# Optimization experiments

Measured on AMD Instinct MI355X. Metric: run time of the kernel, lower is better.

The kernel has to match this reference:

```python
import jax, jax.numpy as jnp
import numpy as np

B, N_WIRES, LAYERS = 256, 14, 3


def _apply_1q(psi, U, w, n):
    # U: [2,2] (shared across batch) or [B,2,2] (per-sample) complex gate on wire w.
    # Wire 0 is the most-significant tensor factor (PennyLane convention).
    Bsz = psi.shape[0]
    p = psi.reshape(Bsz, 2 ** w, 2, 2 ** (n - w - 1))
    sub = 'bij,bljr->blir' if U.ndim == 3 else 'ij,bljr->blir'
    return jnp.einsum(sub, U, p).reshape(Bsz, -1)


def _apply_rz(psi, theta, w, n):
    # RZ is diagonal: multiply by exp(-i*theta/2), exp(+i*theta/2) on wire w.
    Bsz = psi.shape[0]
    p = psi.reshape(Bsz, 2 ** w, 2, 2 ** (n - w - 1))
    ph = jnp.stack([jnp.exp(-0.5j * theta), jnp.exp(0.5j * theta)])
    return (p * ph[None, None, :, None]).reshape(Bsz, -1)


def _apply_cnot(psi, c, n):
    # CNOT on adjacent wires (control=c, target=c+1): flip target where control=1.
    Bsz = psi.shape[0]
    p = psi.reshape(Bsz, 2 ** c, 2, 2, 2 ** (n - c - 2))
    p = jnp.concatenate([p[:, :, 0:1], p[:, :, 1:2, ::-1]], axis=2)
    return p.reshape(Bsz, -1)


def _circuit(state_batch, var_params):
    Bsz, n = state_batch.shape
    layers = var_params.shape[0]
    psi = jnp.zeros((Bsz, 2 ** n), jnp.complex64).at[:, 0].set(1.0)
    # --- RX encoding with per-sample angles ---
    half = 0.5 * state_batch
    c = jnp.cos(half).astype(jnp.complex64)
    s = (-1j) * jnp.sin(half).astype(jnp.complex64)
    for w in range(n):
        U = jnp.stack([jnp.stack([c[:, w], s[:, w]], -1),
                       jnp.stack([s[:, w], c[:, w]], -1)], -2)  # [B,2,2]
        psi = _apply_1q(psi, U, w, n)
    # --- variational layers: RY, RZ per wire, then CNOT chain ---
    for l in range(layers):
        for w in range(n):
            a = var_params[l, w, 0]
            ca, sa = jnp.cos(0.5 * a), jnp.sin(0.5 * a)
            RY = jnp.stack([jnp.stack([ca, -sa]),
                            jnp.stack([sa, ca])]).astype(jnp.complex64)
            psi = _apply_1q(psi, RY, w, n)
            psi = _apply_rz(psi, var_params[l, w, 1], w, n)
        for i in range(n - 1):
            psi = _apply_cnot(psi, i, n)
    # --- <Z_w> for each wire via signed probability sums ---
    probs = (psi * jnp.conj(psi)).real  # [B, 2^n]
    bits = (np.arange(2 ** n)[None, :] >> (n - 1 - np.arange(n))[:, None]) & 1
    signs = jnp.asarray(1.0 - 2.0 * bits, dtype=probs.dtype)  # [n, 2^n]
    return probs @ signs.T  # [B, n]


def setup_inputs() -> dict:
    key = jax.random.key(0)
    k1, k2, k3 = jax.random.split(key, 3)
    return {
        'state_batch': jax.random.normal(k1, (B, N_WIRES), dtype=jnp.float32),
        'var_params': jax.random.normal(k2, (LAYERS, N_WIRES, 3), dtype=jnp.float32),
        'head_w': jax.random.normal(k3, (1, N_WIRES), dtype=jnp.float32) * 0.25,
        'head_b': jnp.zeros((1,), dtype=jnp.float32),
    }


def reference(state_batch, var_params, head_w, head_b):
    z = _circuit(state_batch, var_params)          # [B, n] PauliZ expectations
    return (z @ head_w.T + head_b)[:, 0]           # Linear(n,1).squeeze(-1) -> [B]
```

## Files before the change

### kernel.cpp

```cpp
#include <hip/hip_runtime.h>


#define NW      14
#define NSTATE  (1 << NW)
#define TPB     1024
#define NLAYERS 3
#define NGATES  (NLAYERS * NW)

typedef float v2f __attribute__((ext_vector_type(2)));

__device__ __forceinline__ int swz(int i) {
    return i ^ ((i >> 4) & 15) ^ ((i >> 8) & 15) ^ ((i >> 9) & 16);
}
__device__ __forceinline__ v2f vswp(v2f a) { return __builtin_shufflevector(a, a, 1, 0); }
__device__ __forceinline__ v2f vspl(float x) { v2f r; r.x = x;  r.y = x; return r; }
__device__ __forceinline__ v2f vpm(float x)  { v2f r; r.x = -x; r.y = x; return r; }
__device__ __forceinline__ float rfl(float x) {
    return __int_as_float(__builtin_amdgcn_readfirstlane(__float_as_int(x)));
}
__device__ __forceinline__ v2f cml(v2f a, v2f b) {
    return vspl(a.x) * b + vpm(a.y) * vswp(b);
}
template <int CTRL>
__device__ __forceinline__ v2f dpp2(v2f a) {
    v2f r;
    r.x = __int_as_float(__builtin_amdgcn_update_dpp(
              0, __float_as_int(a.x), CTRL, 0xF, 0xF, true));
    r.y = __int_as_float(__builtin_amdgcn_update_dpp(
              0, __float_as_int(a.y), CTRL, 0xF, 0xF, true));
    return r;
}

__device__ __forceinline__ void pgp(v2f& a, v2f& d,
                                    float x00, float y00, float x01, float y01,
                                    float x10, float y10, float x11, float y11) {
    const v2f sa = vswp(a), sd = vswp(d);
    const v2f na = vspl(x00) * a + vpm(y00) * sa + vspl(x01) * d + vpm(y01) * sd;
    const v2f nd = vspl(x10) * a + vpm(y10) * sa + vspl(x11) * d + vpm(y11) * sd;
    a = na; d = nd;
}
__device__ __forceinline__ void pgr(v2f& a, v2f& d,
                                    float x00, float x01, float x10, float x11) {
    const v2f na = vspl(x00) * a + vspl(x01) * d;
    const v2f nd = vspl(x10) * a + vspl(x11) * d;
    a = na; d = nd;
}

#define GATE_SGPR(pre, g) \
    const float4 pre##A = gt4[2*(g)], pre##B = gt4[2*(g)+1]; \
    const float pre##0 = rfl(pre##A.x), pre##1 = rfl(pre##A.y), \
                pre##2 = rfl(pre##A.z), pre##3 = rfl(pre##A.w), \
                pre##4 = rfl(pre##B.x), pre##5 = rfl(pre##B.y), \
                pre##6 = rfl(pre##B.z), pre##7 = rfl(pre##B.w);

#define PGP(a, d, pre) pgp(a, d, pre##0,pre##1,pre##2,pre##3, pre##4,pre##5,pre##6,pre##7)
#define PGR(a, d, pre) pgr(a, d, pre##0,pre##2,pre##4,pre##6)

#define LGC1(aX, CT) { const v2f p_ = dpp2<CT>(aX); \
    aX = vspl(cox)*aX + vpm(coy)*vswp(aX) + vspl(cpx)*p_ + vpm(cpy)*vswp(p_); }
#define LGC_ALL(CT) \
    LGC1(a0,CT) LGC1(a1,CT) LGC1(a2,CT) LGC1(a3,CT) \
    LGC1(a4,CT) LGC1(a5,CT) LGC1(a6,CT) LGC1(a7,CT) \
    LGC1(a8,CT) LGC1(a9,CT) LGC1(aA,CT) LGC1(aB,CT) \
    LGC1(aC,CT) LGC1(aD,CT) LGC1(aE,CT) LGC1(aF,CT)
#define LGR1(aX, CT) { const v2f p_ = dpp2<CT>(aX); \
    aX = vspl(cor)*aX + vspl(cpr)*p_; }
#define LGR_ALL(CT) \
    LGR1(a0,CT) LGR1(a1,CT) LGR1(a2,CT) LGR1(a3,CT) \
    LGR1(a4,CT) LGR1(a5,CT) LGR1(a6,CT) LGR1(a7,CT) \
    LGR1(a8,CT) LGR1(a9,CT) LGR1(aA,CT) LGR1(aB,CT) \
    LGR1(aC,CT) LGR1(aD,CT) LGR1(aE,CT) LGR1(aF,CT)

#define MEAS(aX, Dn, par) { \
    const float m_ = ((Dn)&8?-h8:h8)+((Dn)&4?-h9:h9)+((Dn)&2?-h10:h10)+((Dn)&1?-h11:h11); \
    const float cf_ = coefHigh + sc*m_ + ((par)? -Wp : Wp); \
    acc += (aX.x*aX.x + aX.y*aX.y)*cf_; }

__global__ void __launch_bounds__(TPB)
qsim_kernel(const float* __restrict__ state_batch,
            const float* __restrict__ var_params,
            const float* __restrict__ head_w,
            const float* __restrict__ head_b,
            float* __restrict__ out)
{
    __shared__ v2f    psi[NSTATE];
    __shared__ float4 gt4[NGATES * 2];
    __shared__ v2f    vws[NW][2];
    __shared__ float  hws[NW];
    __shared__ float  red[TPB / 64];

    const int t    = threadIdx.x;
    const int lane = t & 63;
    const int wave = t >> 6;
    const int b    = blockIdx.x;

    if (t < NW) {
        float sx, cx, sy, cy, sz, cz;
        sincosf(0.5f * state_batch[b * NW + t], &sx, &cx);
        sincosf(0.5f * var_params[t * 3 + 0], &sy, &cy);
        sincosf(0.5f * var_params[t * 3 + 1], &sz, &cz);
        const float tr = cy * cx, ti = sy * sx;
        const float br = sy * cx, bi = -cy * sx;
        v2f v0, v1;
        v0.x = cz * tr + sz * ti;  v0.y = cz * ti - sz * tr;
        v1.x = cz * br - sz * bi;  v1.y = cz * bi + sz * br;
        vws[t][0] = v0; vws[t][1] = v1;
    }
    if (t >= 64 && t < 64 + NGATES) {
        const int g = t - 64;
        if (g >= NW) {
            float sa, ca, sz, cz;
            sincosf(0.5f * var_params[g * 3 + 0], &sa, &ca);
            if (g >= 2 * NW) { sz = 0.f; cz = 1.f; }
            else sincosf(0.5f * var_params[g * 3 + 1], &sz, &cz);
            gt4[2*g]   = make_float4( ca * cz, -ca * sz, -sa * cz,  sa * sz);
            gt4[2*g+1] = make_float4( sa * cz,  sa * sz,  ca * cz,  ca * sz);
        }
    }
    if (t >= 128 && t < 128 + NW) hws[t - 128] = head_w[t - 128];
    __syncthreads();

    float acc = 0.f;

#pragma unroll 1
    for (int l = 1; l < NLAYERS; ++l) {
        const int g0 = l * NW;
#pragma unroll 1
        for (int p = 0; p < 3; ++p) {
            const int SB = 10 - 4 * p;
            const int LO = 1 << SB;
            const int S0 = swz(LO), S1 = swz(LO << 1);
            const int S2 = swz(LO << 2), S3 = swz(LO << 3);
            const int M  = S3 ^ S2 ^ S1 ^ S0;
            const int gw = g0 + 4 * p;
            GATE_SGPR(ga, gw); GATE_SGPR(gb, gw + 1);
            GATE_SGPR(gc, gw + 2); GATE_SGPR(gd, gw + 3);

            const int i0 = ((t >> SB) << (SB + 4)) | (t & (LO - 1));
            const int s  = swz(i0);

            v2f a0, a1, a2, a3, a4, a5, a6, a7;
            v2f a8, a9, aA, aB, aC, aD, aE, aF;
            if (l == 1 && p == 0) {
                v2f base = cml(vws[5][((t >> 8) ^ (t >> 9)) & 1],
                               vws[6][((t >> 7) ^ (t >> 8)) & 1]);
                v2f m2   = cml(vws[7][((t >> 6) ^ (t >> 7)) & 1],
                               vws[8][((t >> 5) ^ (t >> 6)) & 1]);
                v2f m3   = cml(vws[9][((t >> 4) ^ (t >> 5)) & 1],
                               vws[10][((t >> 3) ^ (t >> 4)) & 1]);
                v2f m4   = cml(vws[11][((t >> 2) ^ (t >> 3)) & 1],
                               vws[12][((t >> 1) ^ (t >> 2)) & 1]);
                base = cml(base, m2);
                m3   = cml(m3, m4);
                base = cml(base, m3);
                base = cml(base, vws[13][(t ^ (t >> 1)) & 1]);
                const int t9 = (t >> 9) & 1;
                const v2f B0 = cml(base, vws[4][t9]);
                const v2f B1 = cml(base, vws[4][t9 ^ 1]);
                const v2f w3B00 = cml(vws[3][0], B0);
                const v2f w3B01 = cml(vws[3][1], B1);
                const v2f w3B10 = cml(vws[3][1], B0);
                const v2f w3B11 = cml(vws[3][0], B1);
                v2f p_, t20, t21;
                p_ = cml(vws[0][0], vws[1][0]);
                t20 = cml(p_, vws[2][0]); t21 = cml(p_, vws[2][1]);
                a0 = cml(t20, w3B00); a1 = cml(t20, w3B01);
                a2 = cml(t21, w3B10); a3 = cml(t21, w3B11);
                p_ = cml(vws[0][0], vws[1][1]);
                t20 = cml(p_, vws[2][1]); t21 = cml(p_, vws[2][0]);
                a4 = cml(t20, w3B00); a5 = cml(t20, w3B01);
                a6 = cml(t21, w3B10); a7 = cml(t21, w3B11);
                p_ = cml(vws[0][1], vws[1][1]);
                t20 = cml(p_, vws[2][0]); t21 = cml(p_, vws[2][1]);
                a8 = cml(t20, w3B00); a9 = cml(t20, w3B01);
                aA = cml(t21, w3B10); aB = cml(t21, w3B11);
                p_ = cml(vws[0][1], vws[1][0]);
                t20 = cml(p_, vws[2][1]); t21 = cml(p_, vws[2][0]);
                aC = cml(t20, w3B00); aD = cml(t20, w3B01);
                aE = cml(t21, w3B10); aF = cml(t21, w3B11);
            } else {
                a0 = psi[s];                a1 = psi[s ^ S0];
                a2 = psi[s ^ S1];           a3 = psi[s ^ S1 ^ S0];
                a4 = psi[s ^ S2];           a5 = psi[s ^ S2 ^ S0];
                a6 = psi[s ^ S2 ^ S1];      a7 = psi[s ^ S2 ^ S1 ^ S0];
                a8 = psi[s ^ S3];           a9 = psi[s ^ S3 ^ S0];
                aA = psi[s ^ S3 ^ S1];      aB = psi[s ^ S3 ^ S1 ^ S0];
                aC = psi[s ^ S3 ^ S2];      aD = psi[s ^ S3 ^ S2 ^ S0];
                aE = psi[s ^ S3 ^ S2 ^ S1]; aF = psi[s ^ M];
            }

            if (l < NLAYERS - 1) {
                PGP(a0, a8, ga); PGP(a1, a9, ga); PGP(a2, aA, ga); PGP(a3, aB, ga);
                PGP(a4, aC, ga); PGP(a5, aD, ga); PGP(a6, aE, ga); PGP(a7, aF, ga);
                PGP(a0, a4, gb); PGP(a1, a5, gb); PGP(a2, a6, gb); PGP(a3, a7, gb);
                PGP(a8, aC, gb); PGP(a9, aD, gb); PGP(aA, aE, gb); PGP(aB, aF, gb);
                PGP(a0, a2, gc); PGP(a1, a3, gc); PGP(a4, a6, gc); PGP(a5, a7, gc);
                PGP(a8, aA, gc); PGP(a9, aB, gc); PGP(aC, aE, gc); PGP(aD, aF, gc);
                PGP(a0, a1, gd); PGP(a2, a3, gd); PGP(a4, a5, gd); PGP(a6, a7, gd);
                PGP(a8, a9, gd); PGP(aA, aB, gd); PGP(aC, aD, gd); PGP(aE, aF, gd);
            } else {
                PGR(a0, a8, ga); PGR(a1, a9, ga); PGR(a2, aA, ga); PGR(a3, aB, ga);
                PGR(a4, aC, ga); PGR(a5, aD, ga); PGR(a6, aE, ga); PGR(a7, aF, ga);
                PGR(a0, a4, gb); PGR(a1, a5, gb); PGR(a2, a6, gb); PGR(a3, a7, gb);
                PGR(a8, aC, gb); PGR(a9, aD, gb); PGR(aA, aE, gb); PGR(aB, aF, gb);
                PGR(a0, a2, gc); PGR(a1, a3, gc); PGR(a4, a6, gc); PGR(a5, a7, gc);
                PGR(a8, aA, gc); PGR(a9, aB, gc); PGR(aC, aE, gc); PGR(aD, aF, gc);
                PGR(a0, a1, gd); PGR(a2, a3, gd); PGR(a4, a5, gd); PGR(a6, a7, gd);
                PGR(a8, a9, gd); PGR(aA, aB, gd); PGR(aC, aD, gd); PGR(aE, aF, gd);
            }

            if (p < 2) {
                const bool cs = ((t >> SB) & 1) != 0;
                const int e = s ^ (cs ? M : 0);
                psi[e]                = a0; psi[e ^ S0]           = a1;
                psi[e ^ S1 ^ S0]      = a2; psi[e ^ S1]           = a3;
                psi[e ^ S2 ^ S1 ^ S0] = a4; psi[e ^ S2 ^ S1]      = a5;
                psi[e ^ S2]           = a6; psi[e ^ S2 ^ S0]      = a7;
                psi[e ^ M]            = a8; psi[e ^ S3 ^ S2 ^ S1] = a9;
                psi[e ^ S3 ^ S2]      = aA; psi[e ^ S3 ^ S2 ^ S0] = aB;
                psi[e ^ S3]           = aC; psi[e ^ S3 ^ S0]      = aD;
                psi[e ^ S3 ^ S1 ^ S0] = aE; psi[e ^ S3 ^ S1]      = aF;
                __syncthreads();
            } else if (l < NLAYERS - 1) {
                GATE_SGPR(gu, g0 + 12);
                GATE_SGPR(gv, g0 + 13);
                {
                    const bool hi = (t & 2) != 0;
                    const float cox = hi ? gu6 : gu0, coy = hi ? gu7 : gu1;
                    const float cpx = hi ? gu4 : gu2, cpy = hi ? gu5 : gu3;
                    LGC_ALL(0x4E)
                }
                {
                    const bool hi = (t & 1) != 0;
                    const float cox = hi ? gv6 : gv0, coy = hi ? gv7 : gv1;
                    const float cpx = hi ? gv4 : gv2, cpy = hi ? gv5 : gv3;
                    LGC_ALL(0xB1)
                }
                const bool cs = ((t >> SB) & 1) != 0;
                const int e = s ^ (cs ? (M ^ 3) : 0) ^ ((t >> 1) & 1);
                psi[e]                    = a0; psi[e ^ S0 ^ 3]           = a1;
                psi[e ^ S1 ^ S0 ^ 3]      = a2; psi[e ^ S1]               = a3;
                psi[e ^ S2 ^ S1 ^ S0 ^ 3] = a4; psi[e ^ S2 ^ S1]          = a5;
                psi[e ^ S2]               = a6; psi[e ^ S2 ^ S0 ^ 3]      = a7;
                psi[e ^ M ^ 3]            = a8; psi[e ^ S3 ^ S2 ^ S1]     = a9;
                psi[e ^ S3 ^ S2]          = aA; psi[e ^ S3 ^ S2 ^ S0 ^ 3] = aB;
                psi[e ^ S3]               = aC; psi[e ^ S3 ^ S0 ^ 3]      = aD;
                psi[e ^ S3 ^ S1 ^ S0 ^ 3] = aE; psi[e ^ S3 ^ S1]          = aF;
                __syncthreads();
            } else {
                GATE_SGPR(gu, g0 + 12);
                GATE_SGPR(gv, g0 + 13);
                {
                    const float cor = gu0;
                    const float cpr = (t & 2) ? gu4 : gu2;
                    LGR_ALL(0x4E)
                }
                {
                    const float cor = gv0;
                    const float cpr = (t & 1) ? gv4 : gv2;
                    LGR_ALL(0xB1)
                }
                const float h8 = hws[8], h9 = hws[9], h10 = hws[10], h11 = hws[11];
                const float h12 = hws[12], h13 = hws[13];
                float coefHigh = 0.f;
#pragma unroll
                for (int j = 0; j < 8; ++j)
                    coefHigh += ((t >> (9 - j)) & 1) ? -hws[j] : hws[j];
                const bool cs = ((t >> SB) & 1) != 0;
                const float sc = cs ? -1.f : 1.f;
                const float w12_0 = (t & 2) ? -h12 : h12;
                const float w13_0 = (((t >> 1) ^ t) & 1) ? -h13 : h13;
                const float Ssum = w12_0 + w13_0;
                const float Wp = cs ? -Ssum : Ssum;
                MEAS(a0, 0, 0)  MEAS(a1, 1, 1)  MEAS(a2, 3, 1)  MEAS(a3, 2, 0)
                MEAS(a4, 7, 1)  MEAS(a5, 6, 0)  MEAS(a6, 4, 0)  MEAS(a7, 5, 1)
                MEAS(a8, 15, 1) MEAS(a9, 14, 0) MEAS(aA, 12, 0) MEAS(aB, 13, 1)
                MEAS(aC, 8, 0)  MEAS(aD, 9, 1)  MEAS(aE, 11, 1) MEAS(aF, 10, 0)
            }
        }
    }

#pragma unroll
    for (int off = 32; off > 0; off >>= 1)
        acc += __shfl_down(acc, off, 64);
    if (lane == 0) red[wave] = acc;
    __syncthreads();
    if (t == 0) {
        float s = 0.f;
#pragma unroll
        for (int i = 0; i < TPB / 64; ++i) s += red[i];
        out[b] = s + head_b[0];
    }
}

extern "C" void kernel_launch(void* const* d_in, const int* in_sizes, int n_in,
                              void* d_out, int out_size, void* d_ws, size_t ws_size,
                              hipStream_t stream) {
    const float* state_batch = (const float*)d_in[0];
    const float* var_params  = (const float*)d_in[1];
    const float* head_w      = (const float*)d_in[2];
    const float* head_b      = (const float*)d_in[3];
    float* out = (float*)d_out;
    qsim_kernel<<<dim3(out_size), dim3(TPB), 0, stream>>>(
        state_batch, var_params, head_w, head_b, out);
}
```

Before: 81.73 us.

## Split fused RY·RZ gates into real RY rotations plus batched diagonal phases

Layer 1's fused complex RY·RZ gate is replaced by a real RY butterfly followed by one combined diagonal phase per amplitude. The phase comes from precomputed tables covering the four wires of each pass, plus a separate table for wires 12 and 13. Because RZ is diagonal and commutes past later RY gates on other wires, the product of RZ phases is applied once per amplitude instead of per gate. This roughly halves the FLOPs of the butterflies but adds extra LDS table reads and per-amplitude complex multiplies, and it relies on the RZ/CNOT ordering being preserved.

```diff
diff --git a/kernel.cpp b/kernel.cpp
--- a/kernel.cpp
+++ b/kernel.cpp
@@ -5,7 +5,6 @@
 #define NSTATE  (1 << NW)
 #define TPB     1024
 #define NLAYERS 3
-#define NGATES  (NLAYERS * NW)
 
 typedef float v2f __attribute__((ext_vector_type(2)));
 
@@ -30,15 +29,6 @@
               0, __float_as_int(a.y), CTRL, 0xF, 0xF, true));
     return r;
 }
-
-__device__ __forceinline__ void pgp(v2f& a, v2f& d,
-                                    float x00, float y00, float x01, float y01,
-                                    float x10, float y10, float x11, float y11) {
-    const v2f sa = vswp(a), sd = vswp(d);
-    const v2f na = vspl(x00) * a + vpm(y00) * sa + vspl(x01) * d + vpm(y01) * sd;
-    const v2f nd = vspl(x10) * a + vpm(y10) * sa + vspl(x11) * d + vpm(y11) * sd;
-    a = na; d = nd;
-}
 __device__ __forceinline__ void pgr(v2f& a, v2f& d,
                                     float x00, float x01, float x10, float x11) {
     const v2f na = vspl(x00) * a + vspl(x01) * d;
@@ -46,23 +36,19 @@
     a = na; d = nd;
 }
 
-#define GATE_SGPR(pre, g) \
-    const float4 pre##A = gt4[2*(g)], pre##B = gt4[2*(g)+1]; \
-    const float pre##0 = rfl(pre##A.x), pre##1 = rfl(pre##A.y), \
-                pre##2 = rfl(pre##A.z), pre##3 = rfl(pre##A.w), \
-                pre##4 = rfl(pre##B.x), pre##5 = rfl(pre##B.y), \
-                pre##6 = rfl(pre##B.z), pre##7 = rfl(pre##B.w);
-
-#define PGP(a, d, pre) pgp(a, d, pre##0,pre##1,pre##2,pre##3, pre##4,pre##5,pre##6,pre##7)
-#define PGR(a, d, pre) pgr(a, d, pre##0,pre##2,pre##4,pre##6)
-
-#define LGC1(aX, CT) { const v2f p_ = dpp2<CT>(aX); \
-    aX = vspl(cox)*aX + vpm(coy)*vswp(aX) + vspl(cpx)*p_ + vpm(cpy)*vswp(p_); }
-#define LGC_ALL(CT) \
-    LGC1(a0,CT) LGC1(a1,CT) LGC1(a2,CT) LGC1(a3,CT) \
-    LGC1(a4,CT) LGC1(a5,CT) LGC1(a6,CT) LGC1(a7,CT) \
-    LGC1(a8,CT) LGC1(a9,CT) LGC1(aA,CT) LGC1(aB,CT) \
-    LGC1(aC,CT) LGC1(aD,CT) LGC1(aE,CT) LGC1(aF,CT)
+#define GATE_R(pre, g) \
+    const float4 pre##V = gtr[g]; \
+    const float pre##0 = rfl(pre##V.x), pre##1 = rfl(pre##V.y), \
+                pre##2 = rfl(pre##V.z), pre##3 = rfl(pre##V.w);
+#define PGR4(a, d, pre) pgr(a, d, pre##0, pre##1, pre##2, pre##3)
+
+#define PH2(aE, aO, k) { \
+    const float4 Z_ = zph4[zb + (k)]; \
+    const float ex_ = rfl(Z_.x), ey_ = rfl(Z_.y); \
+    const float ox_ = rfl(Z_.z), oy_ = rfl(Z_.w); \
+    aE = vspl(ex_)*aE + vpm(ey_)*vswp(aE); \
+    aO = vspl(ox_)*aO + vpm(oy_)*vswp(aO); }
+
 #define LGR1(aX, CT) { const v2f p_ = dpp2<CT>(aX); \
     aX = vspl(cor)*aX + vspl(cpr)*p_; }
 #define LGR_ALL(CT) \
@@ -70,6 +56,11 @@
     LGR1(a4,CT) LGR1(a5,CT) LGR1(a6,CT) LGR1(a7,CT) \
     LGR1(a8,CT) LGR1(a9,CT) LGR1(aA,CT) LGR1(aB,CT) \
     LGR1(aC,CT) LGR1(aD,CT) LGR1(aE,CT) LGR1(aF,CT)
+
+#define ETA(aX) { aX = vspl(et.x)*aX + vpm(et.y)*vswp(aX); }
+#define ETA_ALL \
+    ETA(a0) ETA(a1) ETA(a2) ETA(a3) ETA(a4) ETA(a5) ETA(a6) ETA(a7) \
+    ETA(a8) ETA(a9) ETA(aA) ETA(aB) ETA(aC) ETA(aD) ETA(aE) ETA(aF)
 
 #define MEAS(aX, Dn, par) { \
     const float m_ = ((Dn)&8?-h8:h8)+((Dn)&4?-h9:h9)+((Dn)&2?-h10:h10)+((Dn)&1?-h11:h11); \
@@ -84,7 +75,9 @@
             float* __restrict__ out)
 {
     __shared__ v2f    psi[NSTATE];
-    __shared__ float4 gt4[NGATES * 2];
+    __shared__ float4 gtr[2 * NW];
+    __shared__ float4 zph4[3 * 8];
+    __shared__ v2f    zph12[4];
     __shared__ v2f    vws[NW][2];
     __shared__ float  hws[NW];
     __shared__ float  red[TPB / 64];
@@ -106,25 +99,42 @@
         v1.x = cz * br - sz * bi;  v1.y = cz * bi + sz * br;
         vws[t][0] = v0; vws[t][1] = v1;
     }
-    if (t >= 64 && t < 64 + NGATES) {
+    if (t >= 64 && t < 64 + 2 * NW) {
         const int g = t - 64;
-        if (g >= NW) {
-            float sa, ca, sz, cz;
-            sincosf(0.5f * var_params[g * 3 + 0], &sa, &ca);
-            if (g >= 2 * NW) { sz = 0.f; cz = 1.f; }
-            else sincosf(0.5f * var_params[g * 3 + 1], &sz, &cz);
-            gt4[2*g]   = make_float4( ca * cz, -ca * sz, -sa * cz,  sa * sz);
-            gt4[2*g+1] = make_float4( sa * cz,  sa * sz,  ca * cz,  ca * sz);
+        float sa, ca;
+        sincosf(0.5f * var_params[(NW + g) * 3 + 0], &sa, &ca);
+        gtr[g] = make_float4(ca, -sa, sa, ca);
+    }
+    if (t >= 128 && t < 128 + NW) hws[t - 128] = head_w[t - 128];
+    if (t >= 192 && t < 240) {
+        const int k = t - 192, p = k >> 4, o = k & 15;
+        float ang = 0.f;
+#pragma unroll
+        for (int j = 0; j < 4; ++j) {
+            const float z = var_params[(NW + 4 * p + j) * 3 + 1];
+            ang += ((o >> (3 - j)) & 1) ? 0.5f * z : -0.5f * z;
         }
-    }
-    if (t >= 128 && t < 128 + NW) hws[t - 128] = head_w[t - 128];
+        float s_, c_; sincosf(ang, &s_, &c_);
+        if (o & 1) { zph4[p * 8 + (o >> 1)].z = c_; zph4[p * 8 + (o >> 1)].w = s_; }
+        else       { zph4[p * 8 + (o >> 1)].x = c_; zph4[p * 8 + (o >> 1)].y = s_; }
+    }
+    if (t >= 240 && t < 244) {
+        const int k2 = t - 240;
+        const float z12 = var_params[(NW + 12) * 3 + 1];
+        const float z13 = var_params[(NW + 13) * 3 + 1];
+        const float ang = ((k2 & 2) ? 0.5f * z12 : -0.5f * z12)
+                        + ((k2 & 1) ? 0.5f * z13 : -0.5f * z13);
+        float s_, c_; sincosf(ang, &s_, &c_);
+        v2f e; e.x = c_; e.y = s_;
+        zph12[k2] = e;
+    }
     __syncthreads();
 
     float acc = 0.f;
 
 #pragma unroll 1
     for (int l = 1; l < NLAYERS; ++l) {
-        const int g0 = l * NW;
+        const int gl = (l - 1) * NW;
 #pragma unroll 1
         for (int p = 0; p < 3; ++p) {
             const int SB = 10 - 4 * p;
@@ -132,9 +142,9 @@
             const int S0 = swz(LO), S1 = swz(LO << 1);
             const int S2 = swz(LO << 2), S3 = swz(LO << 3);
             const int M  = S3 ^ S2 ^ S1 ^ S0;
-            const int gw = g0 + 4 * p;
-            GATE_SGPR(ga, gw); GATE_SGPR(gb, gw + 1);
-            GATE_SGPR(gc, gw + 2); GATE_SGPR(gd, gw + 3);
+            const int zb = p * 8;
+            GATE_R(ga, gl + 4 * p);     GATE_R(gb, gl + 4 * p + 1);
+            GATE_R(gc, gl + 4 * p + 2); GATE_R(gd, gl + 4 * p + 3);
 
             const int i0 = ((t >> SB) << (SB + 4)) | (t & (LO - 1));
             const int s  = swz(i0);
@@ -189,24 +199,18 @@
                 aE = psi[s ^ S3 ^ S2 ^ S1]; aF = psi[s ^ M];
             }
 
-            if (l < NLAYERS - 1) {
-                PGP(a0, a8, ga); PGP(a1, a9, ga); PGP(a2, aA, ga); PGP(a3, aB, ga);
-                PGP(a4, aC, ga); PGP(a5, aD, ga); PGP(a6, aE, ga); PGP(a7, aF, ga);
-                PGP(a0, a4, gb); PGP(a1, a5, gb); PGP(a2, a6, gb); PGP(a3, a7, gb);
-                PGP(a8, aC, gb); PGP(a9, aD, gb); PGP(aA, aE, gb); PGP(aB, aF, gb);
-                PGP(a0, a2, gc); PGP(a1, a3, gc); PGP(a4, a6, gc); PGP(a5, a7, gc);
-                PGP(a8, aA, gc); PGP(a9, aB, gc); PGP(aC, aE, gc); PGP(aD, aF, gc);
-                PGP(a0, a1, gd); PGP(a2, a3, gd); PGP(a4, a5, gd); PGP(a6, a7, gd);
-                PGP(a8, a9, gd); PGP(aA, aB, gd); PGP(aC, aD, gd); PGP(aE, aF, gd);
-            } else {
-                PGR(a0, a8, ga); PGR(a1, a9, ga); PGR(a2, aA, ga); PGR(a3, aB, ga);
-                PGR(a4, aC, ga); PGR(a5, aD, ga); PGR(a6, aE, ga); PGR(a7, aF, ga);
-                PGR(a0, a4, gb); PGR(a1, a5, gb); PGR(a2, a6, gb); PGR(a3, a7, gb);
-                PGR(a8, aC, gb); PGR(a9, aD, gb); PGR(aA, aE, gb); PGR(aB, aF, gb);
-                PGR(a0, a2, gc); PGR(a1, a3, gc); PGR(a4, a6, gc); PGR(a5, a7, gc);
-                PGR(a8, aA, gc); PGR(a9, aB, gc); PGR(aC, aE, gc); PGR(aD, aF, gc);
-                PGR(a0, a1, gd); PGR(a2, a3, gd); PGR(a4, a5, gd); PGR(a6, a7, gd);
-                PGR(a8, a9, gd); PGR(aA, aB, gd); PGR(aC, aD, gd); PGR(aE, aF, gd);
+            PGR4(a0, a8, ga); PGR4(a1, a9, ga); PGR4(a2, aA, ga); PGR4(a3, aB, ga);
+            PGR4(a4, aC, ga); PGR4(a5, aD, ga); PGR4(a6, aE, ga); PGR4(a7, aF, ga);
+            PGR4(a0, a4, gb); PGR4(a1, a5, gb); PGR4(a2, a6, gb); PGR4(a3, a7, gb);
+            PGR4(a8, aC, gb); PGR4(a9, aD, gb); PGR4(aA, aE, gb); PGR4(aB, aF, gb);
+            PGR4(a0, a2, gc); PGR4(a1, a3, gc); PGR4(a4, a6, gc); PGR4(a5, a7, gc);
+            PGR4(a8, aA, gc); PGR4(a9, aB, gc); PGR4(aC, aE, gc); PGR4(aD, aF, gc);
+            PGR4(a0, a1, gd); PGR4(a2, a3, gd); PGR4(a4, a5, gd); PGR4(a6, a7, gd);
+            PGR4(a8, a9, gd); PGR4(aA, aB, gd); PGR4(aC, aD, gd); PGR4(aE, aF, gd);
+
+            if (l == 1) {
+                PH2(a0, a1, 0) PH2(a2, a3, 1) PH2(a4, a5, 2) PH2(a6, a7, 3)
+                PH2(a8, a9, 4) PH2(aA, aB, 5) PH2(aC, aD, 6) PH2(aE, aF, 7)
             }
 
             if (p < 2) {
@@ -222,20 +226,19 @@
                 psi[e ^ S3 ^ S1 ^ S0] = aE; psi[e ^ S3 ^ S1]      = aF;
                 __syncthreads();
             } else if (l < NLAYERS - 1) {
-                GATE_SGPR(gu, g0 + 12);
-                GATE_SGPR(gv, g0 + 13);
+                GATE_R(gu, gl + 12);
+                GATE_R(gv, gl + 13);
                 {
-                    const bool hi = (t & 2) != 0;
-                    const float cox = hi ? gu6 : gu0, coy = hi ? gu7 : gu1;
-                    const float cpx = hi ? gu4 : gu2, cpy = hi ? gu5 : gu3;
-                    LGC_ALL(0x4E)
+                    const float cor = gu0;
+                    const float cpr = (t & 2) ? gu2 : gu1;
+                    LGR_ALL(0x4E)
                 }
                 {
-                    const bool hi = (t & 1) != 0;
-                    const float cox = hi ? gv6 : gv0, coy = hi ? gv7 : gv1;
-                    const float cpx = hi ? gv4 : gv2, cpy = hi ? gv5 : gv3;
-                    LGC_ALL(0xB1)
+                    const float cor = gv0;
+                    const float cpr = (t & 1) ? gv2 : gv1;
+                    LGR_ALL(0xB1)
                 }
+                { const v2f et = zph12[t & 3]; ETA_ALL }
                 const bool cs = ((t >> SB) & 1) != 0;
                 const int e = s ^ (cs ? (M ^ 3) : 0) ^ ((t >> 1) & 1);
                 psi[e]                    = a0; psi[e ^ S0 ^ 3]           = a1;
@@ -248,16 +251,16 @@
                 psi[e ^ S3 ^ S1 ^ S0 ^ 3] = aE; psi[e ^ S3 ^ S1]          = aF;
                 __syncthreads();
             } else {
-                GATE_SGPR(gu, g0 + 12);
-                GATE_SGPR(gv, g0 + 13);
+                GATE_R(gu, gl + 12);
+                GATE_R(gv, gl + 13);
                 {
                     const float cor = gu0;
-                    const float cpr = (t & 2) ? gu4 : gu2;
+                    const float cpr = (t & 2) ? gu2 : gu1;
                     LGR_ALL(0x4E)
                 }
                 {
                     const float cor = gv0;
-                    const float cpr = (t & 1) ? gv4 : gv2;
+                    const float cpr = (t & 1) ? gv2 : gv1;
                     LGR_ALL(0xB1)
                 }
                 const float h8 = hws[8], h9 = hws[9], h10 = hws[10], h11 = hws[11];
```

New measurement: 79.26 us. 1.03x faster.
